# Performance work log

Measured on AMD Instinct MI355X. Metric: run time of the kernel, lower is better.

Reference implementation:

```python
import jax, jax.numpy as jnp
import numpy as np

L, N, M = 128, 512, 256   # batch-like dim, recurrence length, feature dim (M_size1)
TK, H = 4, 8              # num_blocks, num_heads
DH = M // H
EPS = 1e-5


def setup_inputs() -> dict:
    key = jax.random.key(0)
    ks = jax.random.split(key, 8)
    s = 0.05  # scale raw-randn params for numerical stability
    return {
        "x": jax.random.normal(ks[0], (L, N, M), jnp.float32),
        "weight": jax.random.normal(ks[1], (M, M), jnp.float32) * s,
        "Wqkv": jax.random.normal(ks[2], (TK, 3, H, DH, M), jnp.float32) * s,
        "Wo": jax.random.normal(ks[3], (TK, M, M), jnp.float32) * s,
        "ln_g": jnp.ones((M,), jnp.float32),
        "ln_b": jnp.zeros((M,), jnp.float32),
        "lnz_g": jnp.ones((M,), jnp.float32),
        "lnz_b": jnp.zeros((M,), jnp.float32),
        "fc1_w": jax.random.normal(ks[4], (4 * M, M), jnp.float32) / np.float32(np.sqrt(M)),
        "fc1_b": jnp.zeros((4 * M,), jnp.float32),
        "fc2_w": jax.random.normal(ks[5], (M, 4 * M), jnp.float32) / np.float32(np.sqrt(4 * M)),
        "fc2_b": jnp.zeros((M,), jnp.float32),
    }


def _ln(x, g, b):
    mu = x.mean(-1, keepdims=True)
    var = x.var(-1, keepdims=True)  # biased variance, as torch LayerNorm
    return (x - mu) * jax.lax.rsqrt(var + EPS) * g + b


def _pos_bias(dtype):
    # bias[j, z]   = sin(j / 10000**(2z/M)) for even z
    # bias[j, z+1] = cos(j / 10000**(2z/M))
    pos = jnp.arange(N, dtype=dtype)                      # j
    z = jnp.arange(0, M, 2, dtype=dtype)                  # even indices
    ang = pos[:, None] / (10000.0 ** (2.0 * z / M))       # (N, M/2)
    return jnp.stack([jnp.sin(ang), jnp.cos(ang)], axis=-1).reshape(N, M)


def reference(x, weight, Wqkv, Wo, ln_g, ln_b, lnz_g, lnz_b, fc1_w, fc1_b, fc2_w, fc2_b):
    # savespace: (L, N, M); positional bias depends only on (j, feature)
    s = jnp.einsum('lm,ijm->ijl', weight, x) + _pos_bias(x.dtype)[None]
    inv_sqrt_dh = np.float32(1.0 / np.sqrt(DH))
    for a in range(TK):
        qkv = jnp.einsum('xhdm,ijm->xijhd', Wqkv[a], _ln(s, ln_g, ln_b))
        q, k, v = qkv[0], qkv[1], qkv[2]                  # each (L, N, H, DH)
        rsa = jnp.einsum('ijhd,ijhd->ijh', q * inv_sqrt_dh, k)
        imv = rsa[..., None] * v                           # (L, N, H, DH)
        imv = jnp.cumsum(imv, axis=1)                      # retention recurrence over j
        s = jnp.einsum('nm,ijm->ijn', Wo[a], imv.reshape(L, N, M)) + s
        s = _ln(s, lnz_g, lnz_b) + s
        h = jax.nn.gelu(s @ fc1_w.T + fc1_b, approximate=False)
        s = h @ fc2_w.T + fc2_b
    return s
```

## Files before the change

### kernel.cpp

```cpp
#include <hip/hip_runtime.h>

typedef unsigned int u32;
typedef unsigned short u16;
typedef _Float16 f16;
typedef __attribute__((ext_vector_type(8))) _Float16 f16x8;
typedef __attribute__((ext_vector_type(4))) float f32x4;
typedef __attribute__((ext_vector_type(4))) u16 u16x4;

#define L_ 128
#define N_ 512
#define M_ 256
#define TK_ 4
#define H_ 8
#define R_ (L_*N_)
#define FF_ 1024

__device__ __forceinline__ u16 f2h(float v){ f16 h=(f16)v; return __builtin_bit_cast(u16,h); }
__device__ __forceinline__ float h2f(u16 b){ return (float)__builtin_bit_cast(f16,b); }
__device__ __forceinline__ f32x4 mfmah(f16x8 a, f16x8 b, f32x4 c){
  return __builtin_amdgcn_mfma_f32_16x16x32_f16(a,b,c,0,0,0);
}
__device__ __forceinline__ float gelu_f(float x){
  float e = __expf(-1.702f*x);
  float r = __builtin_amdgcn_rcpf(e + 1.f);
  return x*r;
}


__global__ void k_bias(float* __restrict__ bias){
  int j = blockIdx.x, l = threadIdx.x;
  int t = l>>1;
  float base = expf(-0.14391156831212757f * (float)t);
  float ang = (float)j * base;
  bias[j*M_ + l] = (l&1) ? cosf(ang) : sinf(ang);
}

__global__ void k_pack(const float* __restrict__ src, u16* __restrict__ dst, int K){
  int b = blockIdx.x; int nk = K>>6; int cg = b/nk, k64 = b%nk;
  int t = threadIdx.x;
  int st = t>>6, g = (t>>4)&3, lr = t&15;
  const float* sp = src + (cg*16+lr)*K + k64*64 + st*32 + g*8;
  f16x8 hv;
  #pragma unroll
  for (int e=0;e<8;e++) hv[e] = (f16)sp[e];
  *(f16x8*)(dst + b*1024 + t*8) = hv;
}

__global__ void k_pack_qkv(const float* __restrict__ w, u16* __restrict__ dst){
  int b = blockIdx.x;
  int a = b/192; int rmn = b%192; int grp = rmn>>2, k64 = rmn&3;
  int hd = grp/6, cidx = grp%6;
  int t = threadIdx.x;
  int st = t>>6, g = (t>>4)&3, lr = t&15;
  int cl = cidx*16 + lr;
  int x = cl>>5, d = cl&31;
  const float* sp = w + (((a*3+x)*H_+hd)*32 + d)*M_ + k64*64 + st*32 + g*8;
  f16x8 hv;
  #pragma unroll
  for (int e=0;e<8;e++) hv[e] = (f16)sp[e];
  *(f16x8*)(dst + b*1024 + t*8) = hv;
}

__device__ __forceinline__ void stageA16(const u16* __restrict__ src, u16* __restrict__ Abuf,
                                         int rowbase, int tid){
  int row = tid>>3, skh = tid&7;
  int k64 = skh>>1, st = skh&1;
  int rg = row>>4, lr = row&15;
  const u16* sp = src + (rowbase+row)*M_ + k64*64 + st*32;
  u16* dp = Abuf + (k64*4+rg)*1024 + st*512 + lr*8;
  #pragma unroll
  for (int gg=0;gg<4;gg++)
    *(uint4*)(dp + gg*128) = *(const uint4*)(sp + gg*8);
}

__global__ __launch_bounds__(512) void k_init(const float* __restrict__ X, const u16* __restrict__ Wf,
    const float* __restrict__ bias, const float* __restrict__ lg, const float* __restrict__ lb,
    float* __restrict__ out, u16* __restrict__ P1){
  __shared__ __align__(16) u16 Abuf[16*1024];
  __shared__ float zs[8][64][2];
  int tid = threadIdx.x;
  int wx = tid>>6, lane = tid&63;
  int g = lane>>4, lr = lane&15;
  int lo = g*128 + lr*8;
  int rowbase = blockIdx.x*64;
  {
    int row = tid>>3, skh = tid&7;
    int k64 = skh>>1, st = skh&1;
    int rg = row>>4, slr = row&15;
    const float* sp = X + (rowbase+row)*M_ + k64*64 + st*32;
    u16* dp = Abuf + (k64*4+rg)*1024 + st*512 + slr*8;
    #pragma unroll
    for (int gg=0;gg<4;gg++){
      f16x8 hv;
      #pragma unroll
      for (int e=0;e<8;e++) hv[e] = (f16)sp[gg*8+e];
      *(f16x8*)(dp + gg*128) = hv;
    }
  }
  __syncthreads();
  f32x4 acc[4][2];
  #pragma unroll
  for (int i=0;i<4;i++){ acc[i][0]=0.f; acc[i][1]=0.f; }
  #pragma unroll
  for (int k64=0;k64<4;k64++)
    #pragma unroll
    for (int st=0;st<2;st++){
      f16x8 a[4], b[2];
      #pragma unroll
      for (int i=0;i<4;i++) a[i] = *(const f16x8*)(Abuf + (k64*4 + i)*1024 + st*512 + lo);
      #pragma unroll
      for (int j=0;j<2;j++) b[j] = *(const f16x8*)(Wf + ((wx*2+j)*4 + k64)*1024 + st*512 + lo);
      #pragma unroll
      for (int i=0;i<4;i++)
        #pragma unroll
        for (int j=0;j<2;j++) acc[i][j] = mfmah(a[i], b[j], acc[i][j]);
    }
  #pragma unroll
  for (int i=0;i<4;i++)
    #pragma unroll
    for (int j=0;j<2;j++)
      #pragma unroll
      for (int r=0;r<4;r++){
        int row = rowbase + i*16 + g*4 + r;
        int col = wx*32 + j*16 + lr;
        acc[i][j][r] += bias[(row & (N_-1))*M_ + col];
        out[row*M_ + col] = acc[i][j][r];
      }
  #pragma unroll
  for (int i=0;i<4;i++)
    #pragma unroll
    for (int r=0;r<4;r++){
      float ps = 0.f, qs = 0.f;
      #pragma unroll
      for (int j=0;j<2;j++){ float t = acc[i][j][r]; ps += t; qs += t*t; }
      ps += __shfl_xor(ps,1); qs += __shfl_xor(qs,1);
      ps += __shfl_xor(ps,2); qs += __shfl_xor(qs,2);
      ps += __shfl_xor(ps,4); qs += __shfl_xor(qs,4);
      ps += __shfl_xor(ps,8); qs += __shfl_xor(qs,8);
      if (lr == 0){
        int rowl = i*16 + g*4 + r;
        zs[wx][rowl][0] = ps;
        zs[wx][rowl][1] = qs;
      }
    }
  __syncthreads();
  #pragma unroll
  for (int i=0;i<4;i++)
    #pragma unroll
    for (int r=0;r<4;r++){
      int rowl = i*16 + g*4 + r;
      float sum=0.f, sq=0.f;
      #pragma unroll
      for (int q=0;q<8;q++){ sum += zs[q][rowl][0]; sq += zs[q][rowl][1]; }
      float mean = sum*(1.f/M_);
      float var  = sq*(1.f/M_) - mean*mean;
      float rstd = rsqrtf(var + 1e-5f);
      int row = rowbase + rowl;
      #pragma unroll
      for (int j=0;j<2;j++){
        int col = wx*32 + j*16 + lr;
        P1[row*M_ + col] = f2h((acc[i][j][r]-mean)*rstd*lg[col] + lb[col]);
      }
    }
}

__global__ __launch_bounds__(512) void k_qkv(const u16* __restrict__ P1, const u16* __restrict__ Wq,
    u16* __restrict__ imv){
  __shared__ __align__(16) u16 Abuf[16*1024];
  int tid = threadIdx.x;
  int hd = tid>>6, lane = tid&63;
  int g = lane>>4, lr = lane&15;
  int lo = g*128 + lr*8;
  int rowbase = blockIdx.x*64;
  stageA16(P1, Abuf, rowbase, tid);
  __syncthreads();
  const u16* Wb = Wq + hd*6*4096;
  const float isd = 0.17677669529663687f;
  float rsa[4][4];
  {
    f32x4 aqk[4][4];
    #pragma unroll
    for (int i=0;i<4;i++)
      #pragma unroll
      for (int c=0;c<4;c++) aqk[i][c] = 0.f;
    #pragma unroll
    for (int k64=0;k64<4;k64++)
      #pragma unroll
      for (int st=0;st<2;st++){
        f16x8 a[4];
        #pragma unroll
        for (int i=0;i<4;i++) a[i] = *(const f16x8*)(Abuf + (k64*4 + i)*1024 + st*512 + lo);
        #pragma unroll
        for (int c=0;c<4;c++){
          f16x8 b = *(const f16x8*)(Wb + (c*4 + k64)*1024 + st*512 + lo);
          #pragma unroll
          for (int i=0;i<4;i++) aqk[i][c] = mfmah(a[i], b, aqk[i][c]);
        }
      }
    #pragma unroll
    for (int i=0;i<4;i++){
      f32x4 p = aqk[i][0]*aqk[i][2] + aqk[i][1]*aqk[i][3];
      #pragma unroll
      for (int r=0;r<4;r++){
        float v = p[r];
        v += __shfl_xor(v,1); v += __shfl_xor(v,2);
        v += __shfl_xor(v,4); v += __shfl_xor(v,8);
        rsa[i][r] = v * isd;
      }
    }
  }
  f32x4 av[4][2];
  #pragma unroll
  for (int i=0;i<4;i++){ av[i][0]=0.f; av[i][1]=0.f; }
  #pragma unroll
  for (int k64=0;k64<4;k64++)
    #pragma unroll
    for (int st=0;st<2;st++){
      f16x8 a[4];
      #pragma unroll
      for (int i=0;i<4;i++) a[i] = *(const f16x8*)(Abuf + (k64*4 + i)*1024 + st*512 + lo);
      #pragma unroll
      for (int c=0;c<2;c++){
        f16x8 b = *(const f16x8*)(Wb + ((4+c)*4 + k64)*1024 + st*512 + lo);
        #pragma unroll
        for (int i=0;i<4;i++) av[i][c] = mfmah(a[i], b, av[i][c]);
      }
    }
  #pragma unroll
  for (int i=0;i<4;i++)
    #pragma unroll
    for (int r=0;r<4;r++){
      int row = rowbase + i*16 + g*4 + r;
      imv[row*M_ + hd*32 + lr]      = f2h(rsa[i][r]*av[i][0][r]);
      imv[row*M_ + hd*32 + 16 + lr] = f2h(rsa[i][r]*av[i][1][r]);
    }
}

__global__ __launch_bounds__(256) void k_scan(const u16* __restrict__ imv, u16* __restrict__ P1){
  __shared__ float tot[4][64];
  int bi = blockIdx.x;
  int i = bi>>2, mc = bi&3;
  int tid = threadIdx.x;
  int ml = tid&63, jc = tid>>6;
  int m = mc*64 + ml;
  int base = i*N_*M_ + jc*128*M_ + m;
  float acc = 0.f;
  for (int jb=0;jb<128;jb+=8){
    float t[8];
    #pragma unroll
    for (int u=0;u<8;u++) t[u] = h2f(imv[base + (jb+u)*M_]);
    #pragma unroll
    for (int u=0;u<8;u++) acc += t[u];
  }
  tot[jc][ml] = acc;
  __syncthreads();
  float pre = 0.f;
  #pragma unroll
  for (int q=0;q<3;q++) if (q<jc) pre += tot[q][ml];
  acc = pre;
  for (int jb=0;jb<128;jb+=8){
    float t[8];
    #pragma unroll
    for (int u=0;u<8;u++) t[u] = h2f(imv[base + (jb+u)*M_]);
    #pragma unroll
    for (int u=0;u<8;u++){ acc += t[u]; P1[base + (jb+u)*M_] = f2h(acc); }
  }
}

__global__ __launch_bounds__(512) void k_wo(u16* __restrict__ P1, const u16* __restrict__ Wf,
    const float* __restrict__ sold, const float* __restrict__ lg, const float* __restrict__ lb){
  __shared__ __align__(16) u16 Abuf[16*1024];
  __shared__ float zs[8][64][2];
  int tid = threadIdx.x;
  int wx = tid>>6, lane = tid&63;
  int g = lane>>4, lr = lane&15;
  int lo = g*128 + lr*8;
  int rowbase = blockIdx.x*64;
  stageA16(P1, Abuf, rowbase, tid);
  __syncthreads();
  f32x4 acc[4][2];
  #pragma unroll
  for (int i=0;i<4;i++){ acc[i][0]=0.f; acc[i][1]=0.f; }
  #pragma unroll
  for (int k64=0;k64<4;k64++)
    #pragma unroll
    for (int st=0;st<2;st++){
      f16x8 a[4], b[2];
      #pragma unroll
      for (int i=0;i<4;i++) a[i] = *(const f16x8*)(Abuf + (k64*4 + i)*1024 + st*512 + lo);
      #pragma unroll
      for (int j=0;j<2;j++) b[j] = *(const f16x8*)(Wf + ((wx*2+j)*4 + k64)*1024 + st*512 + lo);
      #pragma unroll
      for (int i=0;i<4;i++)
        #pragma unroll
        for (int j=0;j<2;j++) acc[i][j] = mfmah(a[i], b[j], acc[i][j]);
    }
  #pragma unroll
  for (int i=0;i<4;i++)
    #pragma unroll
    for (int j=0;j<2;j++)
      #pragma unroll
      for (int r=0;r<4;r++){
        int row = rowbase + i*16 + g*4 + r;
        int col = wx*32 + j*16 + lr;
        acc[i][j][r] += sold[row*M_ + col];
      }
  #pragma unroll
  for (int i=0;i<4;i++)
    #pragma unroll
    for (int r=0;r<4;r++){
      float ps = 0.f, qs = 0.f;
      #pragma unroll
      for (int j=0;j<2;j++){ float t = acc[i][j][r]; ps += t; qs += t*t; }
      ps += __shfl_xor(ps,1); qs += __shfl_xor(qs,1);
      ps += __shfl_xor(ps,2); qs += __shfl_xor(qs,2);
      ps += __shfl_xor(ps,4); qs += __shfl_xor(qs,4);
      ps += __shfl_xor(ps,8); qs += __shfl_xor(qs,8);
      if (lr == 0){
        int rowl = i*16 + g*4 + r;
        zs[wx][rowl][0] = ps;
        zs[wx][rowl][1] = qs;
      }
    }
  __syncthreads();
  #pragma unroll
  for (int i=0;i<4;i++)
    #pragma unroll
    for (int r=0;r<4;r++){
      int rowl = i*16 + g*4 + r;
      float sum=0.f, sq=0.f;
      #pragma unroll
      for (int q=0;q<8;q++){ sum += zs[q][rowl][0]; sq += zs[q][rowl][1]; }
      float mean = sum*(1.f/M_);
      float var  = sq*(1.f/M_) - mean*mean;
      float rstd = rsqrtf(var + 1e-5f);
      int row = rowbase + rowl;
      #pragma unroll
      for (int j=0;j<2;j++){
        int col = wx*32 + j*16 + lr;
        float zv = acc[i][j][r];
        P1[row*M_ + col] = f2h((zv-mean)*rstd*lg[col] + lb[col] + zv);
      }
    }
}

__global__ __launch_bounds__(512) void k_fc(u16* __restrict__ P1,
    const u16* __restrict__ W1f, const float* __restrict__ b1,
    const u16* __restrict__ W2f, const float* __restrict__ b2,
    const float* __restrict__ lg, const float* __restrict__ lb,
    float* __restrict__ out){
  __shared__ __align__(16) u16 Abuf[16*1024];
  __shared__ __align__(16) u16 Hbuf[64*128];
  __shared__ float zs[8][64][2];
  int tid = threadIdx.x;
  int wx = tid>>6, lane = tid&63;
  int g = lane>>4, lr = lane&15;
  int lo = g*128 + lr*8;
  int rowbase = blockIdx.x*64;
  stageA16(P1, Abuf, rowbase, tid);
  __syncthreads();
  f32x4 acc2[4][2];
  #pragma unroll
  for (int i=0;i<4;i++){ acc2[i][0]=0.f; acc2[i][1]=0.f; }
  for (int c=0;c<8;c++){
    f32x4 acc1[4];
    #pragma unroll
    for (int j=0;j<4;j++) acc1[j] = 0.f;
    #pragma unroll
    for (int k64=0;k64<4;k64++)
      #pragma unroll
      for (int st=0;st<2;st++){
        f16x8 aw = *(const f16x8*)(W1f + ((c*8 + wx)*4 + k64)*1024 + st*512 + lo);
        #pragma unroll
        for (int j=0;j<4;j++){
          f16x8 bs = *(const f16x8*)(Abuf + (k64*4 + j)*1024 + st*512 + lo);
          acc1[j] = mfmah(aw, bs, acc1[j]);
        }
      }
    __syncthreads();
    {
      int fl = wx*16 + g*4;
      int kc = fl>>6, kloc = fl&63;
      float4 b1v = *(const float4*)(b1 + c*128 + fl);
      float bb[4] = {b1v.x, b1v.y, b1v.z, b1v.w};
      #pragma unroll
      for (int j=0;j<4;j++){
        int row = j*16 + lr;
        u16x4 hv;
        #pragma unroll
        for (int r=0;r<4;r++)
          hv[r] = f2h(gelu_f(acc1[j][r] + bb[r]));
        int phys = ((kloc>>3) ^ row) & 7;
        *(u16x4*)(Hbuf + row*128 + kc*64 + phys*8 + (kloc&7)) = hv;
      }
    }
    __syncthreads();
    #pragma unroll
    for (int kcl=0;kcl<2;kcl++)
      #pragma unroll
      for (int st=0;st<2;st++){
        f16x8 ah[4], bb2[2];
        #pragma unroll
        for (int j=0;j<2;j++)
          bb2[j] = *(const f16x8*)(W2f + ((wx*2+j)*16 + c*2 + kcl)*1024 + st*512 + lo);
        #pragma unroll
        for (int i=0;i<4;i++){
          int hrow = i*16 + lr;
          int phys = (((st<<2)|g) ^ hrow) & 7;
          ah[i] = *(const f16x8*)(Hbuf + hrow*128 + kcl*64 + phys*8);
        }
        #pragma unroll
        for (int i=0;i<4;i++)
          #pragma unroll
          for (int j=0;j<2;j++) acc2[i][j] = mfmah(ah[i], bb2[j], acc2[i][j]);
      }
  }
  #pragma unroll
  for (int i=0;i<4;i++)
    #pragma unroll
    for (int j=0;j<2;j++)
      #pragma unroll
      for (int r=0;r<4;r++){
        int row = rowbase + i*16 + g*4 + r;
        int col = wx*32 + j*16 + lr;
        acc2[i][j][r] += b2[col];
        out[row*M_ + col] = acc2[i][j][r];
      }
  #pragma unroll
  for (int i=0;i<4;i++)
    #pragma unroll
    for (int r=0;r<4;r++){
      float ps = 0.f, qs = 0.f;
      #pragma unroll
      for (int j=0;j<2;j++){ float t = acc2[i][j][r]; ps += t; qs += t*t; }
      ps += __shfl_xor(ps,1); qs += __shfl_xor(qs,1);
      ps += __shfl_xor(ps,2); qs += __shfl_xor(qs,2);
      ps += __shfl_xor(ps,4); qs += __shfl_xor(qs,4);
      ps += __shfl_xor(ps,8); qs += __shfl_xor(qs,8);
      if (lr == 0){
        int rowl = i*16 + g*4 + r;
        zs[wx][rowl][0] = ps;
        zs[wx][rowl][1] = qs;
      }
    }
  __syncthreads();
  #pragma unroll
  for (int i=0;i<4;i++)
    #pragma unroll
    for (int r=0;r<4;r++){
      int rowl = i*16 + g*4 + r;
      float sum=0.f, sq=0.f;
      #pragma unroll
      for (int q=0;q<8;q++){ sum += zs[q][rowl][0]; sq += zs[q][rowl][1]; }
      float mean = sum*(1.f/M_);
      float var  = sq*(1.f/M_) - mean*mean;
      float rstd = rsqrtf(var + 1e-5f);
      int row = rowbase + rowl;
      #pragma unroll
      for (int j=0;j<2;j++){
        int col = wx*32 + j*16 + lr;
        P1[row*M_ + col] = f2h((acc2[i][j][r]-mean)*rstd*lg[col] + lb[col]);
      }
    }
}

extern "C" void kernel_launch(void* const* d_in, const int* in_sizes, int n_in,
                              void* d_out, int out_size, void* d_ws, size_t ws_size,
                              hipStream_t stream){
  const float* x      = (const float*)d_in[0];
  const float* weight = (const float*)d_in[1];
  const float* wqkv   = (const float*)d_in[2];
  const float* wo     = (const float*)d_in[3];
  const float* ln_g   = (const float*)d_in[4];
  const float* ln_b   = (const float*)d_in[5];
  const float* lnz_g  = (const float*)d_in[6];
  const float* lnz_b  = (const float*)d_in[7];
  const float* fc1_w  = (const float*)d_in[8];
  const float* fc1_b  = (const float*)d_in[9];
  const float* fc2_w  = (const float*)d_in[10];
  const float* fc2_b  = (const float*)d_in[11];
  float* out = (float*)d_out;
  char* ws = (char*)d_ws;
  size_t off = 0;
  u16* wqkvf   = (u16*)(ws + off); off += 1572864;
  u16* wof     = (u16*)(ws + off); off += 524288;
  u16* fc1f    = (u16*)(ws + off); off += 524288;
  u16* fc2f    = (u16*)(ws + off); off += 524288;
  u16* weightf = (u16*)(ws + off); off += 131072;
  float* bias  = (float*)(ws + off); off += 524288;
  u16* P1      = (u16*)(ws + off); off += 33554432;
  u16* imv     = (u16*)(ws + off); off += 33554432;

  k_bias<<<N_, M_, 0, stream>>>(bias);
  k_pack<<<64, 128, 0, stream>>>(weight, weightf, 256);
  k_pack_qkv<<<768, 128, 0, stream>>>(wqkv, wqkvf);
  k_pack<<<256, 128, 0, stream>>>(wo, wof, 256);
  k_pack<<<256, 128, 0, stream>>>(fc1_w, fc1f, 256);
  k_pack<<<256, 128, 0, stream>>>(fc2_w, fc2f, 1024);
  k_init<<<R_/64, 512, 0, stream>>>(x, weightf, bias, ln_g, ln_b, out, P1);
  for (int a=0; a<TK_; a++){
    k_qkv<<<R_/64, 512, 0, stream>>>(P1, wqkvf + a*196608, imv);
    k_scan<<<L_*4, 256, 0, stream>>>(imv, P1);
    k_wo<<<R_/64, 512, 0, stream>>>(P1, wof + a*65536, out, lnz_g, lnz_b);
    k_fc<<<R_/64, 512, 0, stream>>>(P1, fc1f, fc1_b, fc2f, fc2_b, ln_g, ln_b, out);
  }
}
```

Baseline: 796.9 us.

## Store activations in MFMA fragment layout and read operands directly from global

The intermediate activation buffer is now written in the tiled fragment order the MFMA operand loads expect, rather than row-major. The qkv, wo and fc kernels drop their LDS staging and barrier and load A fragments straight from global memory as 16-byte vectors. This removes the per-block shared-memory copy and sync and frees LDS. The cost is repeated global/L2 reads of the same fragments across waves, and scattered 2-byte stores in the scan and epilogues.

```diff
diff --git a/kernel.cpp b/kernel.cpp
--- a/kernel.cpp
+++ b/kernel.cpp
@@ -26,6 +26,9 @@
   return x*r;
 }
 
+__device__ __forceinline__ int p1a(int row, int col){
+  return (row>>4)*4096 + (col>>6)*1024 + ((col>>5)&1)*512 + ((col>>3)&3)*128 + (row&15)*8 + (col&7);
+}
 
 __global__ void k_bias(float* __restrict__ bias){
   int j = blockIdx.x, l = threadIdx.x;
@@ -61,21 +64,9 @@
   *(f16x8*)(dst + b*1024 + t*8) = hv;
 }
 
-__device__ __forceinline__ void stageA16(const u16* __restrict__ src, u16* __restrict__ Abuf,
-                                         int rowbase, int tid){
-  int row = tid>>3, skh = tid&7;
-  int k64 = skh>>1, st = skh&1;
-  int rg = row>>4, lr = row&15;
-  const u16* sp = src + (rowbase+row)*M_ + k64*64 + st*32;
-  u16* dp = Abuf + (k64*4+rg)*1024 + st*512 + lr*8;
-  #pragma unroll
-  for (int gg=0;gg<4;gg++)
-    *(uint4*)(dp + gg*128) = *(const uint4*)(sp + gg*8);
-}
-
 __global__ __launch_bounds__(512) void k_init(const float* __restrict__ X, const u16* __restrict__ Wf,
     const float* __restrict__ bias, const float* __restrict__ lg, const float* __restrict__ lb,
-    float* __restrict__ out, u16* __restrict__ P1){
+    float* __restrict__ out, u16* __restrict__ P1f){
   __shared__ __align__(16) u16 Abuf[16*1024];
   __shared__ float zs[8][64][2];
   int tid = threadIdx.x;
@@ -159,21 +150,19 @@
       #pragma unroll
       for (int j=0;j<2;j++){
         int col = wx*32 + j*16 + lr;
-        P1[row*M_ + col] = f2h((acc[i][j][r]-mean)*rstd*lg[col] + lb[col]);
-      }
-    }
-}
-
-__global__ __launch_bounds__(512) void k_qkv(const u16* __restrict__ P1, const u16* __restrict__ Wq,
+        P1f[p1a(row,col)] = f2h((acc[i][j][r]-mean)*rstd*lg[col] + lb[col]);
+      }
+    }
+}
+
+__global__ __launch_bounds__(512) void k_qkv(const u16* __restrict__ P1f, const u16* __restrict__ Wq,
     u16* __restrict__ imv){
-  __shared__ __align__(16) u16 Abuf[16*1024];
   int tid = threadIdx.x;
   int hd = tid>>6, lane = tid&63;
   int g = lane>>4, lr = lane&15;
   int lo = g*128 + lr*8;
   int rowbase = blockIdx.x*64;
-  stageA16(P1, Abuf, rowbase, tid);
-  __syncthreads();
+  const u16* Ab = P1f + (rowbase>>4)*4096;
   const u16* Wb = Wq + hd*6*4096;
   const float isd = 0.17677669529663687f;
   float rsa[4][4];
@@ -189,7 +178,7 @@
       for (int st=0;st<2;st++){
         f16x8 a[4];
         #pragma unroll
-        for (int i=0;i<4;i++) a[i] = *(const f16x8*)(Abuf + (k64*4 + i)*1024 + st*512 + lo);
+        for (int i=0;i<4;i++) a[i] = *(const f16x8*)(Ab + i*4096 + k64*1024 + st*512 + lo);
         #pragma unroll
         for (int c=0;c<4;c++){
           f16x8 b = *(const f16x8*)(Wb + (c*4 + k64)*1024 + st*512 + lo);
@@ -218,7 +207,7 @@
     for (int st=0;st<2;st++){
       f16x8 a[4];
       #pragma unroll
-      for (int i=0;i<4;i++) a[i] = *(const f16x8*)(Abuf + (k64*4 + i)*1024 + st*512 + lo);
+      for (int i=0;i<4;i++) a[i] = *(const f16x8*)(Ab + i*4096 + k64*1024 + st*512 + lo);
       #pragma unroll
       for (int c=0;c<2;c++){
         f16x8 b = *(const f16x8*)(Wb + ((4+c)*4 + k64)*1024 + st*512 + lo);
@@ -236,7 +225,7 @@
     }
 }
 
-__global__ __launch_bounds__(256) void k_scan(const u16* __restrict__ imv, u16* __restrict__ P1){
+__global__ __launch_bounds__(256) void k_scan(const u16* __restrict__ imv, u16* __restrict__ P1f){
   __shared__ float tot[4][64];
   int bi = blockIdx.x;
   int i = bi>>2, mc = bi&3;
@@ -244,6 +233,7 @@
   int ml = tid&63, jc = tid>>6;
   int m = mc*64 + ml;
   int base = i*N_*M_ + jc*128*M_ + m;
+  int rowbase = i*N_ + jc*128;
   float acc = 0.f;
   for (int jb=0;jb<128;jb+=8){
     float t[8];
@@ -263,21 +253,19 @@
     #pragma unroll
     for (int u=0;u<8;u++) t[u] = h2f(imv[base + (jb+u)*M_]);
     #pragma unroll
-    for (int u=0;u<8;u++){ acc += t[u]; P1[base + (jb+u)*M_] = f2h(acc); }
-  }
-}
-
-__global__ __launch_bounds__(512) void k_wo(u16* __restrict__ P1, const u16* __restrict__ Wf,
+    for (int u=0;u<8;u++){ acc += t[u]; P1f[p1a(rowbase + jb + u, m)] = f2h(acc); }
+  }
+}
+
+__global__ __launch_bounds__(512) void k_wo(u16* __restrict__ P1f, const u16* __restrict__ Wf,
     const float* __restrict__ sold, const float* __restrict__ lg, const float* __restrict__ lb){
-  __shared__ __align__(16) u16 Abuf[16*1024];
   __shared__ float zs[8][64][2];
   int tid = threadIdx.x;
   int wx = tid>>6, lane = tid&63;
   int g = lane>>4, lr = lane&15;
   int lo = g*128 + lr*8;
   int rowbase = blockIdx.x*64;
-  stageA16(P1, Abuf, rowbase, tid);
-  __syncthreads();
+  const u16* Ab = P1f + (rowbase>>4)*4096;
   f32x4 acc[4][2];
   #pragma unroll
   for (int i=0;i<4;i++){ acc[i][0]=0.f; acc[i][1]=0.f; }
@@ -287,7 +275,7 @@
     for (int st=0;st<2;st++){
       f16x8 a[4], b[2];
       #pragma unroll
-      for (int i=0;i<4;i++) a[i] = *(const f16x8*)(Abuf + (k64*4 + i)*1024 + st*512 + lo);
+      for (int i=0;i<4;i++) a[i] = *(const f16x8*)(Ab + i*4096 + k64*1024 + st*512 + lo);
       #pragma unroll
       for (int j=0;j<2;j++) b[j] = *(const f16x8*)(Wf + ((wx*2+j)*4 + k64)*1024 + st*512 + lo);
       #pragma unroll
@@ -339,17 +327,16 @@
       for (int j=0;j<2;j++){
         int col = wx*32 + j*16 + lr;
         float zv = acc[i][j][r];
-        P1[row*M_ + col] = f2h((zv-mean)*rstd*lg[col] + lb[col] + zv);
-      }
-    }
-}
-
-__global__ __launch_bounds__(512) void k_fc(u16* __restrict__ P1,
+        P1f[p1a(row,col)] = f2h((zv-mean)*rstd*lg[col] + lb[col] + zv);
+      }
+    }
+}
+
+__global__ __launch_bounds__(512) void k_fc(u16* __restrict__ P1f,
     const u16* __restrict__ W1f, const float* __restrict__ b1,
     const u16* __restrict__ W2f, const float* __restrict__ b2,
     const float* __restrict__ lg, const float* __restrict__ lb,
     float* __restrict__ out){
-  __shared__ __align__(16) u16 Abuf[16*1024];
   __shared__ __align__(16) u16 Hbuf[64*128];
   __shared__ float zs[8][64][2];
   int tid = threadIdx.x;
@@ -357,8 +344,7 @@
   int g = lane>>4, lr = lane&15;
   int lo = g*128 + lr*8;
   int rowbase = blockIdx.x*64;
-  stageA16(P1, Abuf, rowbase, tid);
-  __syncthreads();
+  const u16* Ab = P1f + (rowbase>>4)*4096;
   f32x4 acc2[4][2];
   #pragma unroll
   for (int i=0;i<4;i++){ acc2[i][0]=0.f; acc2[i][1]=0.f; }
@@ -373,7 +359,7 @@
         f16x8 aw = *(const f16x8*)(W1f + ((c*8 + wx)*4 + k64)*1024 + st*512 + lo);
         #pragma unroll
         for (int j=0;j<4;j++){
-          f16x8 bs = *(const f16x8*)(Abuf + (k64*4 + j)*1024 + st*512 + lo);
+          f16x8 bs = *(const f16x8*)(Ab + j*4096 + k64*1024 + st*512 + lo);
           acc1[j] = mfmah(aw, bs, acc1[j]);
         }
       }
@@ -459,7 +445,7 @@
       #pragma unroll
       for (int j=0;j<2;j++){
         int col = wx*32 + j*16 + lr;
-        P1[row*M_ + col] = f2h((acc2[i][j][r]-mean)*rstd*lg[col] + lb[col]);
+        P1f[p1a(row,col)] = f2h((acc2[i][j][r]-mean)*rstd*lg[col] + lb[col]);
       }
     }
 }
@@ -488,7 +474,7 @@
   u16* fc2f    = (u16*)(ws + off); off += 524288;
   u16* weightf = (u16*)(ws + off); off += 131072;
   float* bias  = (float*)(ws + off); off += 524288;
-  u16* P1      = (u16*)(ws + off); off += 33554432;
+  u16* P1f     = (u16*)(ws + off); off += 33554432;
   u16* imv     = (u16*)(ws + off); off += 33554432;
 
   k_bias<<<N_, M_, 0, stream>>>(bias);
@@ -497,11 +483,11 @@
   k_pack<<<256, 128, 0, stream>>>(wo, wof, 256);
   k_pack<<<256, 128, 0, stream>>>(fc1_w, fc1f, 256);
   k_pack<<<256, 128, 0, stream>>>(fc2_w, fc2f, 1024);
-  k_init<<<R_/64, 512, 0, stream>>>(x, weightf, bias, ln_g, ln_b, out, P1);
+  k_init<<<R_/64, 512, 0, stream>>>(x, weightf, bias, ln_g, ln_b, out, P1f);
   for (int a=0; a<TK_; a++){
-    k_qkv<<<R_/64, 512, 0, stream>>>(P1, wqkvf + a*196608, imv);
-    k_scan<<<L_*4, 256, 0, stream>>>(imv, P1);
-    k_wo<<<R_/64, 512, 0, stream>>>(P1, wof + a*65536, out, lnz_g, lnz_b);
-    k_fc<<<R_/64, 512, 0, stream>>>(P1, fc1f, fc1_b, fc2f, fc2_b, ln_g, ln_b, out);
-  }
-}
+    k_qkv<<<R_/64, 512, 0, stream>>>(P1f, wqkvf + a*196608, imv);
+    k_scan<<<L_*4, 256, 0, stream>>>(imv, P1f);
+    k_wo<<<R_/64, 512, 0, stream>>>(P1f, wof + a*65536, out, lnz_g, lnz_b);
+    k_fc<<<R_/64, 512, 0, stream>>>(P1f, fc1f, fc1_b, fc2f, fc2_b, ln_g, ln_b, out);
+  }
+}
```

New measurement: 1.103 ms. +38.4%, slower.
